# Optimization experiments

Hardware: AMD Instinct MI355X
Metric: run time of the kernel (lower is better)

Reference implementation:

```python
import jax, jax.numpy as jnp
import numpy as np

N_NODES = 200_000
N_EDGES = 6_400_000
N_GRAPHS = 512


def _graph_conv(x, src, dst, W_rel, b_rel, W_root, n_nodes):
    # PyG GraphConv (aggr='add'): lin_rel(sum_{j->i} x_j) + lin_root(x_i)
    agg = jax.ops.segment_sum(x[src], dst, num_segments=n_nodes)  # [N, in]
    return agg @ W_rel.T + b_rel + x @ W_root.T


def setup_inputs() -> dict:
    key = jax.random.key(0)
    ks = jax.random.split(key, 12)
    x = jax.random.normal(ks[0], (N_NODES, 3), dtype=jnp.float32)
    edge_index = jax.random.randint(ks[1], (2, N_EDGES), 0, N_NODES, dtype=jnp.int64)
    batch = jnp.sort(jax.random.randint(ks[2], (N_NODES,), 0, N_GRAPHS, dtype=jnp.int64))

    def xavier(k, shape):
        fan_out, fan_in = shape
        lim = np.sqrt(6.0 / (fan_in + fan_out)).astype(np.float32)
        return jax.random.uniform(k, shape, jnp.float32, -lim, lim)

    return {
        "x": x, "edge_index": edge_index, "batch": batch,
        "W1_rel": xavier(ks[3], (32, 3)),  "b1": jnp.zeros((32,), jnp.float32), "W1_root": xavier(ks[4], (32, 3)),
        "W2_rel": xavier(ks[5], (16, 32)), "b2": jnp.zeros((16,), jnp.float32), "W2_root": xavier(ks[6], (16, 32)),
        "W3_rel": xavier(ks[7], (8, 16)),  "b3": jnp.zeros((8,), jnp.float32),  "W3_root": xavier(ks[8], (8, 16)),
        "W_lin": xavier(ks[9], (1, 8)),    "b_lin": jnp.zeros((1,), jnp.float32),
    }


def reference(x, edge_index, batch,
              W1_rel, b1, W1_root,
              W2_rel, b2, W2_root,
              W3_rel, b3, W3_root,
              W_lin, b_lin):
    src, dst = edge_index[0], edge_index[1]
    h = jax.nn.relu(_graph_conv(x, src, dst, W1_rel, b1, W1_root, N_NODES))
    h = jax.nn.relu(_graph_conv(h, src, dst, W2_rel, b2, W2_root, N_NODES))
    h = jax.nn.relu(_graph_conv(h, src, dst, W3_rel, b3, W3_root, N_NODES))
    pooled = jax.ops.segment_max(h, batch, num_segments=N_GRAPHS)  # [G, 8]
    out = pooled @ W_lin.T + b_lin  # [G, 1]
    return out[:, 0]
```

## Files before the change

### kernel.cpp

```cpp
#include <hip/hip_runtime.h>
#include <hip/hip_fp16.h>

#define N_NODES 200000
#define N_EDGES 6400000
#define N_GRAPHS 512

#define NB1 196
#define CB 1024
#define NSB 16
#define NFB (NB1 * NSB)
#define CHUNK 8192
#define NCH 782
#define NGRP 25
#define CPG 32
#define SCAP 3072

typedef float vf4 __attribute__((ext_vector_type(4)));
typedef float vf2 __attribute__((ext_vector_type(2)));
typedef unsigned vu2 __attribute__((ext_vector_type(2)));

__device__ __forceinline__ unsigned ntload_u(const unsigned* p) {
  return __builtin_nontemporal_load(p);
}
__device__ __forceinline__ int ntload_i(const int* p) { return __builtin_nontemporal_load(p); }
__device__ __forceinline__ float ntload_f(const float* p) {
  return __builtin_nontemporal_load(p);
}
__device__ __forceinline__ float2 ntload_f2(const float* p) {
  vf2 v = __builtin_nontemporal_load((const vf2*)p);
  return make_float2(v.x, v.y);
}
__device__ __forceinline__ void ntstore_f2(float* p, float2 v) {
  vf2 t = {v.x, v.y};
  __builtin_nontemporal_store(t, (vf2*)p);
}
__device__ __forceinline__ void ntstore_u(unsigned* p, unsigned v) {
  __builtin_nontemporal_store(v, p);
}


__global__ __launch_bounds__(256) void count_kernel(const int* __restrict__ dst,
                                                    unsigned short* __restrict__ H) {
  __shared__ unsigned hist[4][NB1];
  int t = threadIdx.x, w = t >> 6;
  for (int i = t; i < 4 * NB1; i += 256) ((unsigned*)hist)[i] = 0;
  __syncthreads();
  int c = blockIdx.x;
  long e0 = (long)c * CHUNK;
  long rem = (long)N_EDGES - e0;
  int n = rem > CHUNK ? CHUNK : (int)rem;
  for (int i = t; i < n; i += 256) atomicAdd(&hist[w][dst[e0 + i] >> 10], 1u);
  __syncthreads();
  for (int b = t; b < NB1; b += 256)
    H[(size_t)c * NB1 + b] =
        (unsigned short)(hist[0][b] + hist[1][b] + hist[2][b] + hist[3][b]);
}

__global__ __launch_bounds__(256) void scan_bins1_kernel(unsigned short* __restrict__ H,
                                                         unsigned* __restrict__ P) {
  int b = blockIdx.x * 256 + threadIdx.x;
  int g = blockIdx.y;
  if (b >= NB1) return;
  int c0 = g * CPG, c1 = min(NCH, (g + 1) * CPG);
  unsigned run = 0;
  for (int c = c0; c < c1; c++) {
    unsigned t = H[(size_t)c * NB1 + b];
    H[(size_t)c * NB1 + b] = (unsigned short)run;
    run += t;
  }
  P[(size_t)g * NB1 + b] = run;
}

__global__ __launch_bounds__(256) void scan_bins2_kernel(unsigned* __restrict__ P,
                                                         unsigned* __restrict__ bucketTotal) {
  int b = blockIdx.x * 256 + threadIdx.x;
  if (b >= NB1) return;
  unsigned run = 0;
  for (int g = 0; g < NGRP; g++) {
    unsigned t = P[(size_t)g * NB1 + b];
    P[(size_t)g * NB1 + b] = run;
    run += t;
  }
  bucketTotal[b] = run;
}

__global__ __launch_bounds__(256) void scan_total_kernel(const unsigned* __restrict__ bucketTotal,
                                                         unsigned* __restrict__ bucketStart) {
  __shared__ unsigned partial[256];
  int t = threadIdx.x;
  unsigned v = (t < NB1) ? bucketTotal[t] : 0u;
  partial[t] = v;
  __syncthreads();
  for (int off = 1; off < 256; off <<= 1) {
    unsigned add = (t >= off) ? partial[t - off] : 0u;
    __syncthreads();
    partial[t] += add;
    __syncthreads();
  }
  if (t < NB1) bucketStart[t] = partial[t] - v;
  if (t == 0) bucketStart[NB1] = N_EDGES;
}

__global__ __launch_bounds__(256) void scatterA_kernel(
    const int* __restrict__ src, const int* __restrict__ dst,
    const unsigned short* __restrict__ H, const unsigned* __restrict__ P,
    const unsigned* __restrict__ bucketStart, unsigned* __restrict__ X1) {
  __shared__ unsigned ssort[CHUNK];
  __shared__ unsigned char sbort[CHUNK];
  __shared__ unsigned histw[4][NB1];
  __shared__ unsigned curw[4][NB1];
  __shared__ unsigned gbase[NB1];
  __shared__ unsigned partial[256];
  int t = threadIdx.x, w = t >> 6;
  int c = blockIdx.x;
  int g = c / CPG;
  long e0 = (long)c * CHUNK;
  long rem = (long)N_EDGES - e0;
  int n = rem > CHUNK ? CHUNK : (int)rem;
  for (int i = t; i < 4 * NB1; i += 256) ((unsigned*)histw)[i] = 0;
  __syncthreads();
  for (int i = t; i < n; i += 256) atomicAdd(&histw[w][dst[e0 + i] >> 10], 1u);
  __syncthreads();
  unsigned tot = 0, h0 = 0, h1 = 0, h2 = 0, h3 = 0;
  if (t < NB1) {
    h0 = histw[0][t]; h1 = histw[1][t]; h2 = histw[2][t]; h3 = histw[3][t];
    tot = h0 + h1 + h2 + h3;
  }
  partial[t] = tot;
  __syncthreads();
  for (int off = 1; off < 256; off <<= 1) {
    unsigned add = (t >= off) ? partial[t - off] : 0u;
    __syncthreads();
    partial[t] += add;
    __syncthreads();
  }
  if (t < NB1) {
    unsigned ex = partial[t] - tot;
    unsigned r = ex;
    curw[0][t] = r; r += h0;
    curw[1][t] = r; r += h1;
    curw[2][t] = r; r += h2;
    curw[3][t] = r;
    gbase[t] = bucketStart[t] + P[(size_t)g * NB1 + t] + (unsigned)H[(size_t)c * NB1 + t] - ex;
  }
  __syncthreads();
  for (int i = t; i < n; i += 256) {
    int d = dst[e0 + i], s = src[e0 + i];
    int b = d >> 10;
    unsigned r = atomicAdd(&curw[w][b], 1u);
    ssort[r] = ((unsigned)s << 10) | (unsigned)(d & 1023);
    sbort[r] = (unsigned char)b;
  }
  __syncthreads();
  for (int j = t; j < n; j += 256) X1[gbase[sbort[j]] + j] = ssort[j];
}

__global__ __launch_bounds__(1024) void scatterB_kernel(
    const unsigned* __restrict__ X1, const unsigned* __restrict__ bucketStart,
    unsigned* __restrict__ X2, unsigned* __restrict__ fineStart) {
  __shared__ unsigned histw[16][NSB];
  __shared__ unsigned binstart[NSB + 1];
  __shared__ unsigned cur[NSB];
  int t = threadIdx.x, w = t >> 6, b = blockIdx.x;
  unsigned cs0 = bucketStart[b], cs1 = bucketStart[b + 1];
  int n = (int)(cs1 - cs0);
  if (t < 16 * NSB) ((unsigned*)histw)[t] = 0;
  __syncthreads();
  for (int i = t; i < n; i += 1024)
    atomicAdd(&histw[w][(X1[cs0 + i] >> 6) & 15u], 1u);
  __syncthreads();
  if (t == 0) {
    unsigned run = 0;
    for (int k = 0; k < NSB; k++) {
      binstart[k] = run;
      unsigned tot = 0;
      for (int ww = 0; ww < 16; ww++) tot += histw[ww][k];
      run += tot;
    }
    binstart[NSB] = run;
  }
  __syncthreads();
  if (t < NSB) {
    fineStart[b * NSB + t] = cs0 + binstart[t];
    cur[t] = binstart[t];
  }
  if (b == NB1 - 1 && t == 0) fineStart[NFB] = cs1;
  __syncthreads();
  for (int i = t; i < n; i += 1024) {
    unsigned v = X1[cs0 + i];
    unsigned pos = atomicAdd(&cur[(v >> 6) & 15u], 1u);
    X2[cs0 + pos] = v;
  }
}

__global__ __launch_bounds__(256) void sort2_kernel(const unsigned* __restrict__ X2,
                                                    const unsigned* __restrict__ fineStart,
                                                    unsigned* __restrict__ packedB,
                                                    unsigned* __restrict__ nodeStart) {
  __shared__ unsigned buf[SCAP];
  __shared__ unsigned buf2[SCAP];
  __shared__ unsigned hist[64], base[64], cur[64];
  int t = threadIdx.x, b = blockIdx.x;
  unsigned s0 = fineStart[b], s1 = fineStart[b + 1];
  int n = (int)(s1 - s0);
  if (t < 64) hist[t] = 0;
  for (int i = t; i < n; i += 256) buf[i] = ntload_u(&X2[s0 + i]);
  __syncthreads();
  for (int i = t; i < n; i += 256) atomicAdd(&hist[buf[i] & 63u], 1u);
  __syncthreads();
  if (t == 0) {
    unsigned run = 0;
    for (int k = 0; k < 64; k++) {
      unsigned v = hist[k];
      base[k] = run;
      cur[k] = run;
      run += v;
    }
  }
  __syncthreads();
  if (t < 64) {
    int gn = b * 64 + t;
    if (gn <= N_NODES) nodeStart[gn] = s0 + base[t];
  }
  for (int i = t; i < n; i += 256) {
    unsigned p = buf[i];
    unsigned pos = atomicAdd(&cur[p & 63u], 1u);
    buf2[pos] = p >> 10;
  }
  __syncthreads();
  for (int i = t; i < n; i += 256) ntstore_u(&packedB[s0 + i], buf2[i]);
}

__global__ __launch_bounds__(256) void xpad_kernel(const float* __restrict__ x,
                                                   float4* __restrict__ xp) {
  int n = blockIdx.x * 256 + threadIdx.x;
  if (n >= N_NODES) return;
  xp[n] = make_float4(x[3 * n], x[3 * n + 1], x[3 * n + 2], 0.f);
}

__device__ __forceinline__ void half8_unpack(uint4 g, float* f) {
  const __half2* h2 = reinterpret_cast<const __half2*>(&g);
#pragma unroll
  for (int j = 0; j < 4; j++) {
    float2 fj = __half22float2(h2[j]);
    f[2 * j] = fj.x;
    f[2 * j + 1] = fj.y;
  }
}

__global__ __launch_bounds__(256) void layer1a_kernel(
    const unsigned* __restrict__ packed, const unsigned* __restrict__ nodeStart,
    const float4* __restrict__ xp, float* __restrict__ agg) {
  int t = threadIdx.x, ln = t >> 2, part = t & 3;
  int node = blockIdx.x * 64 + ln;
  unsigned s1v = ntload_u(&nodeStart[node + 1]);
  float a0 = 0.f, a1 = 0.f, a2 = 0.f;
  for (unsigned base = ntload_u(&nodeStart[node]) + part; base < s1v; base += 16) {
    unsigned i1 = base + 4, i2 = base + 8, i3 = base + 12;
    unsigned e0 = ntload_u(&packed[base]);
    unsigned e1 = ntload_u(&packed[i1]);
    unsigned e2 = ntload_u(&packed[i2]);
    unsigned e3 = ntload_u(&packed[i3]);
    float4 g0 = xp[e0], g1 = xp[e1], g2 = xp[e2], g3 = xp[e3];
    float m1 = (i1 < s1v) ? 1.f : 0.f;
    float m2 = (i2 < s1v) ? 1.f : 0.f;
    float m3 = (i3 < s1v) ? 1.f : 0.f;
    a0 += g0.x + m1 * g1.x + m2 * g2.x + m3 * g3.x;
    a1 += g0.y + m1 * g1.y + m2 * g2.y + m3 * g3.y;
    a2 += g0.z + m1 * g1.z + m2 * g2.z + m3 * g3.z;
  }
  a0 += __shfl_xor(a0, 1); a1 += __shfl_xor(a1, 1); a2 += __shfl_xor(a2, 1);
  a0 += __shfl_xor(a0, 2); a1 += __shfl_xor(a1, 2); a2 += __shfl_xor(a2, 2);
  float v = (part == 0) ? a0 : (part == 1) ? a1 : (part == 2) ? a2 : 0.f;
  agg[(size_t)node * 4 + part] = v;
}

__global__ __launch_bounds__(256) void layer1b_kernel(
    const float4* __restrict__ xp, const float4* __restrict__ agg,
    const float* __restrict__ W1_rel, const float* __restrict__ b1,
    const float* __restrict__ W1_root,
    const float* __restrict__ W2_rel, const float* __restrict__ W2_root,
    uint4* __restrict__ t2h4, float4* __restrict__ r24) {
  __shared__ float sW1rel[96], sW1root[96], sb1[32], sW2rel[512], sW2root[512];
  for (int i = threadIdx.x; i < 96; i += 256) { sW1rel[i] = W1_rel[i]; sW1root[i] = W1_root[i]; }
  for (int i = threadIdx.x; i < 32; i += 256) sb1[i] = b1[i];
  for (int i = threadIdx.x; i < 512; i += 256) { sW2rel[i] = W2_rel[i]; sW2root[i] = W2_root[i]; }
  __syncthreads();
  int node = blockIdx.x * 256 + threadIdx.x;
  if (node >= N_NODES) return;
  float4 A = agg[node];
  float4 xv = xp[node];
  float h[32];
#pragma unroll
  for (int k = 0; k < 32; k++) {
    float v = sW1rel[3 * k] * A.x + sW1rel[3 * k + 1] * A.y + sW1rel[3 * k + 2] * A.z +
              sW1root[3 * k] * xv.x + sW1root[3 * k + 1] * xv.y + sW1root[3 * k + 2] * xv.z +
              sb1[k];
    h[k] = fmaxf(v, 0.f);
  }
  unsigned tp[8];
#pragma unroll
  for (int j = 0; j < 16; j += 2) {
    float t0 = 0.f, t1 = 0.f;
#pragma unroll
    for (int k = 0; k < 32; k++) {
      t0 += sW2rel[32 * j + k] * h[k];
      t1 += sW2rel[32 * (j + 1) + k] * h[k];
    }
    __half2 pk = __halves2half2(__float2half_rn(t0), __float2half_rn(t1));
    tp[j >> 1] = *(unsigned*)&pk;
  }
  t2h4[(size_t)node * 2] = make_uint4(tp[0], tp[1], tp[2], tp[3]);
  t2h4[(size_t)node * 2 + 1] = make_uint4(tp[4], tp[5], tp[6], tp[7]);
#pragma unroll
  for (int q = 0; q < 4; q++) {
    float rv[4];
#pragma unroll
    for (int jj = 0; jj < 4; jj++) {
      int j = 4 * q + jj;
      float a = 0.f;
#pragma unroll
      for (int k = 0; k < 32; k++) a += sW2root[32 * j + k] * h[k];
      rv[jj] = a;
    }
    r24[(size_t)node * 4 + q] = make_float4(rv[0], rv[1], rv[2], rv[3]);
  }
}

__global__ __launch_bounds__(256) void layer2_kernel(
    const unsigned* __restrict__ packed, const unsigned* __restrict__ nodeStart,
    const uint4* __restrict__ t2h4, const float* __restrict__ r2,
    const float* __restrict__ b2,
    const float* __restrict__ W3_rel, const float* __restrict__ W3_root,
    unsigned* __restrict__ t3h, float* __restrict__ r3) {
  __shared__ float sW3rel[128], sW3root[128], sb2[16];
  __shared__ float plds[256 * 9];
  __shared__ float hlds[32 * 16];
  for (int i = threadIdx.x; i < 128; i += 256) { sW3rel[i] = W3_rel[i]; sW3root[i] = W3_root[i]; }
  if (threadIdx.x < 16) sb2[threadIdx.x] = b2[threadIdx.x];
  __syncthreads();
  int t = threadIdx.x, ln = t >> 3, p = t & 7;
  int node = blockIdx.x * 32 + ln;
  int half = p & 1;
  unsigned s1v = ntload_u(&nodeStart[node + 1]);
  float acc[8];
#pragma unroll
  for (int j = 0; j < 8; j++) acc[j] = 0.f;
  for (unsigned base = ntload_u(&nodeStart[node]) + (p >> 1); base < s1v; base += 16) {
    unsigned i1 = base + 4, i2 = base + 8, i3 = base + 12;
    unsigned e0 = ntload_u(&packed[base]);
    unsigned e1 = ntload_u(&packed[i1]);
    unsigned e2 = ntload_u(&packed[i2]);
    unsigned e3 = ntload_u(&packed[i3]);
    uint4 g0 = t2h4[(size_t)e0 * 2 + half];
    uint4 g1 = t2h4[(size_t)e1 * 2 + half];
    uint4 g2 = t2h4[(size_t)e2 * 2 + half];
    uint4 g3 = t2h4[(size_t)e3 * 2 + half];
    float m1 = (i1 < s1v) ? 1.f : 0.f;
    float m2 = (i2 < s1v) ? 1.f : 0.f;
    float m3 = (i3 < s1v) ? 1.f : 0.f;
    float f0[8], f1[8], f2[8], f3[8];
    half8_unpack(g0, f0);
    half8_unpack(g1, f1);
    half8_unpack(g2, f2);
    half8_unpack(g3, f3);
#pragma unroll
    for (int j = 0; j < 8; j++)
      acc[j] += f0[j] + m1 * f1[j] + m2 * f2[j] + m3 * f3[j];
  }
#pragma unroll
  for (int j = 0; j < 8; j++) plds[t * 9 + j] = acc[j];
  __syncthreads();
  {
    float2 rv = ntload_f2(&r2[(size_t)node * 16 + 2 * p]);
    float hv[2];
#pragma unroll
    for (int k2 = 0; k2 < 2; k2++) {
      int f = 2 * p + k2;
      int fh = f >> 3, fi = f & 7;
      int q0 = (ln * 8 + fh) * 9 + fi;
      float s = plds[q0] + plds[q0 + 18] + plds[q0 + 36] + plds[q0 + 54];
      hv[k2] = s + sb2[f] + (k2 == 0 ? rv.x : rv.y);
    }
    hlds[ln * 16 + 2 * p] = fmaxf(hv[0], 0.f);
    hlds[ln * 16 + 2 * p + 1] = fmaxf(hv[1], 0.f);
  }
  __syncthreads();
  const float* W = (p < 4) ? sW3rel : sW3root;
  int rbase = (p < 4) ? 2 * p : 2 * (p - 4);
  float o0 = 0.f, o1 = 0.f;
#pragma unroll
  for (int k = 0; k < 16; k++) {
    float hv = hlds[ln * 16 + k];
    o0 += W[16 * rbase + k] * hv;
    o1 += W[16 * (rbase + 1) + k] * hv;
  }
  if (p < 4) {
    __half2 pk = __halves2half2(__float2half_rn(o0), __float2half_rn(o1));
    t3h[(size_t)node * 4 + p] = *(unsigned*)&pk;
  } else {
    ntstore_f2(&r3[(size_t)node * 8 + rbase], make_float2(o0, o1));
  }
}

__global__ __launch_bounds__(256) void layer3_kernel(
    const unsigned* __restrict__ packed, const unsigned* __restrict__ nodeStart,
    const uint4* __restrict__ t3h4, const float* __restrict__ r3,
    const float* __restrict__ b3,
    const int* __restrict__ batch, unsigned* __restrict__ pooled) {
  __shared__ float plds[256 * 9];
  __shared__ float sb3[8];
  __shared__ int sgid[32];
  if (threadIdx.x < 8) sb3[threadIdx.x] = b3[threadIdx.x];
  __syncthreads();
  int t = threadIdx.x, ln = t >> 3, p = t & 7;
  int node = blockIdx.x * 32 + ln;
  unsigned s1v = ntload_u(&nodeStart[node + 1]);
  float acc[8];
#pragma unroll
  for (int j = 0; j < 8; j++) acc[j] = 0.f;
  for (unsigned base = ntload_u(&nodeStart[node]) + p; base < s1v; base += 32) {
    unsigned i1 = base + 8, i2 = base + 16, i3 = base + 24;
    unsigned e0 = ntload_u(&packed[base]);
    unsigned e1 = ntload_u(&packed[i1]);
    unsigned e2 = ntload_u(&packed[i2]);
    unsigned e3 = ntload_u(&packed[i3]);
    uint4 g0 = t3h4[e0];
    uint4 g1 = t3h4[e1];
    uint4 g2 = t3h4[e2];
    uint4 g3 = t3h4[e3];
    float m1 = (i1 < s1v) ? 1.f : 0.f;
    float m2 = (i2 < s1v) ? 1.f : 0.f;
    float m3 = (i3 < s1v) ? 1.f : 0.f;
    float f0[8], f1[8], f2[8], f3[8];
    half8_unpack(g0, f0);
    half8_unpack(g1, f1);
    half8_unpack(g2, f2);
    half8_unpack(g3, f3);
#pragma unroll
    for (int j = 0; j < 8; j++)
      acc[j] += f0[j] + m1 * f1[j] + m2 * f2[j] + m3 * f3[j];
  }
#pragma unroll
  for (int j = 0; j < 8; j++) plds[t * 9 + j] = acc[j];
  __syncthreads();
  int gg = ntload_i(&batch[node]);
  int q0 = ln * 72 + p;
  float v = plds[q0] + plds[q0 + 9] + plds[q0 + 18] + plds[q0 + 27] +
            plds[q0 + 36] + plds[q0 + 45] + plds[q0 + 54] + plds[q0 + 63];
  float h = fmaxf(v + sb3[p] + ntload_f(&r3[(size_t)node * 8 + p]), 0.f);
  __syncthreads();
  plds[ln * 9 + p] = h;
  if (p == 0) sgid[ln] = gg;
  __syncthreads();
  if (t < 8) {
    int gcur = sgid[0];
    float m = plds[t];
    for (int l = 1; l < 32; l++) {
      int g2 = sgid[l];
      float hv = plds[l * 9 + t];
      if (g2 != gcur) {
        atomicMax(&pooled[8 * gcur + t], __float_as_uint(m));
        gcur = g2;
        m = hv;
      } else {
        m = fmaxf(m, hv);
      }
    }
    atomicMax(&pooled[8 * gcur + t], __float_as_uint(m));
  }
}

__global__ __launch_bounds__(256) void final_kernel(
    const unsigned* __restrict__ pooled, const float* __restrict__ W_lin,
    const float* __restrict__ b_lin, float* __restrict__ out) {
  int g = blockIdx.x * blockDim.x + threadIdx.x;
  if (g >= N_GRAPHS) return;
  float acc = b_lin[0];
#pragma unroll
  for (int f = 0; f < 8; f++) acc += __uint_as_float(pooled[8 * g + f]) * W_lin[f];
  out[g] = acc;
}

extern "C" void kernel_launch(void* const* d_in, const int* in_sizes, int n_in,
                              void* d_out, int out_size, void* d_ws, size_t ws_size,
                              hipStream_t stream) {
  const float* x = (const float*)d_in[0];
  const int* ei = (const int*)d_in[1];
  const int* src = ei;
  const int* dst = ei + N_EDGES;
  const int* batch = (const int*)d_in[2];
  const float* W1_rel = (const float*)d_in[3];
  const float* b1 = (const float*)d_in[4];
  const float* W1_root = (const float*)d_in[5];
  const float* W2_rel = (const float*)d_in[6];
  const float* b2 = (const float*)d_in[7];
  const float* W2_root = (const float*)d_in[8];
  const float* W3_rel = (const float*)d_in[9];
  const float* b3 = (const float*)d_in[10];
  const float* W3_root = (const float*)d_in[11];
  const float* W_lin = (const float*)d_in[12];
  const float* b_lin = (const float*)d_in[13];
  float* out = (float*)d_out;

  char* ws = (char*)d_ws;
  unsigned* X2 = (unsigned*)(ws + 0);
  float* r2 = (float*)(ws + 0);
  float* agg = (float*)(ws + 12800000);
  float* r3 = (float*)(ws + 12800000);
  unsigned* t3h = (unsigned*)(ws + 19200000);
  float4* xpad = (float4*)(ws + 22400000);
  unsigned* X1 = (unsigned*)(ws + 25600000);
  unsigned* packedB = (unsigned*)(ws + 25600000);
  unsigned* t2h = (unsigned*)(ws + 51200128);
  unsigned short* H = (unsigned short*)(ws + 51200128);
  unsigned* P = (unsigned*)(ws + 51506672);
  unsigned* bucketTotal = (unsigned*)(ws + 51526272);
  unsigned* bucketStart = (unsigned*)(ws + 51527056);
  unsigned* fineStart = (unsigned*)(ws + 51527844);
  unsigned* pooled = (unsigned*)(ws + 57600128);
  unsigned* nodeStart = (unsigned*)(ws + 57954016);

  hipMemsetAsync(pooled, 0, N_GRAPHS * 8 * sizeof(unsigned), stream);
  hipMemsetAsync(packedB + N_EDGES, 0, 128, stream);

  count_kernel<<<NCH, 256, 0, stream>>>(dst, H);
  scan_bins1_kernel<<<dim3((NB1 + 255) / 256, NGRP), 256, 0, stream>>>(H, P);
  scan_bins2_kernel<<<(NB1 + 255) / 256, 256, 0, stream>>>(P, bucketTotal);
  scan_total_kernel<<<1, 256, 0, stream>>>(bucketTotal, bucketStart);
  scatterA_kernel<<<NCH, 256, 0, stream>>>(src, dst, H, P, bucketStart, X1);
  scatterB_kernel<<<NB1, 1024, 0, stream>>>(X1, bucketStart, X2, fineStart);
  sort2_kernel<<<NFB, 256, 0, stream>>>(X2, fineStart, packedB, nodeStart);
  xpad_kernel<<<(N_NODES + 255) / 256, 256, 0, stream>>>(x, xpad);

  layer1a_kernel<<<N_NODES / 64, 256, 0, stream>>>(packedB, nodeStart, xpad, agg);
  layer1b_kernel<<<(N_NODES + 255) / 256, 256, 0, stream>>>(
      xpad, (const float4*)agg, W1_rel, b1, W1_root, W2_rel, W2_root,
      (uint4*)t2h, (float4*)r2);
  layer2_kernel<<<N_NODES / 32, 256, 0, stream>>>(packedB, nodeStart, (const uint4*)t2h, r2, b2,
                                                  W3_rel, W3_root, t3h, r3);
  layer3_kernel<<<N_NODES / 32, 256, 0, stream>>>(packedB, nodeStart, (const uint4*)t3h, r3, b3,
                                                  batch, pooled);
  final_kernel<<<(N_GRAPHS + 255) / 256, 256, 0, stream>>>(pooled, W_lin, b_lin, out);
}
```

Baseline: 429.0 us.

## Split layer-2 gather by feature half and move epilogue to separate kernel

Layer 2 is split into two kernels. The gather kernel now has each block handle only one 8-feature half of the 16-wide half-precision table, with blocks ordered so both halves of the same node group run close together. Each thread walks every 8th edge and the block writes fp16 partial aggregates. A separate elementwise kernel then applies bias, residual and ReLU, and computes the layer-3 projections. The aim is to shrink the gathered footprint per block and improve cache locality, at the cost of reading the edge list twice, one extra launch and an fp16 round-trip of the aggregate.

```diff
diff --git a/kernel.cpp b/kernel.cpp
--- a/kernel.cpp
+++ b/kernel.cpp
@@ -14,6 +14,7 @@
 #define NGRP 25
 #define CPG 32
 #define SCAP 3072
+#define NBLK32 (N_NODES / 32)
 
 typedef float vf4 __attribute__((ext_vector_type(4)));
 typedef float vf2 __attribute__((ext_vector_type(2)));
@@ -327,27 +328,22 @@
   }
 }
 
-__global__ __launch_bounds__(256) void layer2_kernel(
+__global__ __launch_bounds__(256) void layer2g_kernel(
     const unsigned* __restrict__ packed, const unsigned* __restrict__ nodeStart,
-    const uint4* __restrict__ t2h4, const float* __restrict__ r2,
-    const float* __restrict__ b2,
-    const float* __restrict__ W3_rel, const float* __restrict__ W3_root,
-    unsigned* __restrict__ t3h, float* __restrict__ r3) {
-  __shared__ float sW3rel[128], sW3root[128], sb2[16];
+    const uint4* __restrict__ t2h4, __half* __restrict__ agg2) {
   __shared__ float plds[256 * 9];
-  __shared__ float hlds[32 * 16];
-  for (int i = threadIdx.x; i < 128; i += 256) { sW3rel[i] = W3_rel[i]; sW3root[i] = W3_root[i]; }
-  if (threadIdx.x < 16) sb2[threadIdx.x] = b2[threadIdx.x];
-  __syncthreads();
   int t = threadIdx.x, ln = t >> 3, p = t & 7;
-  int node = blockIdx.x * 32 + ln;
-  int half = p & 1;
+  int b = blockIdx.x;
+  int r = b & 7, half = r & 1, sub = r >> 1;
+  int nodeblk = (b >> 3) * 4 + sub;
+  if (nodeblk >= NBLK32) return;
+  int node = nodeblk * 32 + ln;
   unsigned s1v = ntload_u(&nodeStart[node + 1]);
   float acc[8];
 #pragma unroll
   for (int j = 0; j < 8; j++) acc[j] = 0.f;
-  for (unsigned base = ntload_u(&nodeStart[node]) + (p >> 1); base < s1v; base += 16) {
-    unsigned i1 = base + 4, i2 = base + 8, i3 = base + 12;
+  for (unsigned base = ntload_u(&nodeStart[node]) + p; base < s1v; base += 32) {
+    unsigned i1 = base + 8, i2 = base + 16, i3 = base + 24;
     unsigned e0 = ntload_u(&packed[base]);
     unsigned e1 = ntload_u(&packed[i1]);
     unsigned e2 = ntload_u(&packed[i2]);
@@ -371,36 +367,59 @@
 #pragma unroll
   for (int j = 0; j < 8; j++) plds[t * 9 + j] = acc[j];
   __syncthreads();
-  {
-    float2 rv = ntload_f2(&r2[(size_t)node * 16 + 2 * p]);
-    float hv[2];
-#pragma unroll
-    for (int k2 = 0; k2 < 2; k2++) {
-      int f = 2 * p + k2;
-      int fh = f >> 3, fi = f & 7;
-      int q0 = (ln * 8 + fh) * 9 + fi;
-      float s = plds[q0] + plds[q0 + 18] + plds[q0 + 36] + plds[q0 + 54];
-      hv[k2] = s + sb2[f] + (k2 == 0 ? rv.x : rv.y);
+  int q0 = ln * 72 + p;
+  float s = plds[q0] + plds[q0 + 9] + plds[q0 + 18] + plds[q0 + 27] +
+            plds[q0 + 36] + plds[q0 + 45] + plds[q0 + 54] + plds[q0 + 63];
+  agg2[(size_t)node * 16 + half * 8 + p] = __float2half_rn(s);
+}
+
+__global__ __launch_bounds__(256) void layer2e_kernel(
+    const uint4* agg2q, const float4* __restrict__ r24,
+    const float* __restrict__ b2, const float* __restrict__ W3_rel,
+    const float* __restrict__ W3_root, uint4* __restrict__ t3h4, float4* r34) {
+  __shared__ float sW3rel[128], sW3root[128], sb2[16];
+  for (int i = threadIdx.x; i < 128; i += 256) { sW3rel[i] = W3_rel[i]; sW3root[i] = W3_root[i]; }
+  if (threadIdx.x < 16) sb2[threadIdx.x] = b2[threadIdx.x];
+  __syncthreads();
+  int node = blockIdx.x * 256 + threadIdx.x;
+  if (node >= N_NODES) return;
+  uint4 ga = agg2q[(size_t)node * 2];
+  uint4 gb = agg2q[(size_t)node * 2 + 1];
+  float ag[16];
+  half8_unpack(ga, ag);
+  half8_unpack(gb, ag + 8);
+  float h[16];
+#pragma unroll
+  for (int q = 0; q < 4; q++) {
+    float4 rv = r24[(size_t)node * 4 + q];
+    h[4 * q] = fmaxf(ag[4 * q] + rv.x + sb2[4 * q], 0.f);
+    h[4 * q + 1] = fmaxf(ag[4 * q + 1] + rv.y + sb2[4 * q + 1], 0.f);
+    h[4 * q + 2] = fmaxf(ag[4 * q + 2] + rv.z + sb2[4 * q + 2], 0.f);
+    h[4 * q + 3] = fmaxf(ag[4 * q + 3] + rv.w + sb2[4 * q + 3], 0.f);
+  }
+  unsigned tp[4];
+#pragma unroll
+  for (int j = 0; j < 8; j += 2) {
+    float t0 = 0.f, t1 = 0.f;
+#pragma unroll
+    for (int k = 0; k < 16; k++) {
+      t0 += sW3rel[16 * j + k] * h[k];
+      t1 += sW3rel[16 * (j + 1) + k] * h[k];
     }
-    hlds[ln * 16 + 2 * p] = fmaxf(hv[0], 0.f);
-    hlds[ln * 16 + 2 * p + 1] = fmaxf(hv[1], 0.f);
-  }
-  __syncthreads();
-  const float* W = (p < 4) ? sW3rel : sW3root;
-  int rbase = (p < 4) ? 2 * p : 2 * (p - 4);
-  float o0 = 0.f, o1 = 0.f;
-#pragma unroll
-  for (int k = 0; k < 16; k++) {
-    float hv = hlds[ln * 16 + k];
-    o0 += W[16 * rbase + k] * hv;
-    o1 += W[16 * (rbase + 1) + k] * hv;
-  }
-  if (p < 4) {
-    __half2 pk = __halves2half2(__float2half_rn(o0), __float2half_rn(o1));
-    t3h[(size_t)node * 4 + p] = *(unsigned*)&pk;
-  } else {
-    ntstore_f2(&r3[(size_t)node * 8 + rbase], make_float2(o0, o1));
-  }
+    __half2 pk = __halves2half2(__float2half_rn(t0), __float2half_rn(t1));
+    tp[j >> 1] = *(unsigned*)&pk;
+  }
+  t3h4[node] = make_uint4(tp[0], tp[1], tp[2], tp[3]);
+  float rv[8];
+#pragma unroll
+  for (int j = 0; j < 8; j++) {
+    float a = 0.f;
+#pragma unroll
+    for (int k = 0; k < 16; k++) a += sW3root[16 * j + k] * h[k];
+    rv[j] = a;
+  }
+  r34[(size_t)node * 2] = make_float4(rv[0], rv[1], rv[2], rv[3]);
+  r34[(size_t)node * 2 + 1] = make_float4(rv[4], rv[5], rv[6], rv[7]);
 }
 
 __global__ __launch_bounds__(256) void layer3_kernel(
@@ -507,6 +526,7 @@
   unsigned* X2 = (unsigned*)(ws + 0);
   float* r2 = (float*)(ws + 0);
   float* agg = (float*)(ws + 12800000);
+  __half* agg2 = (__half*)(ws + 12800000);
   float* r3 = (float*)(ws + 12800000);
   unsigned* t3h = (unsigned*)(ws + 19200000);
   float4* xpad = (float4*)(ws + 22400000);
@@ -537,8 +557,13 @@
   layer1b_kernel<<<(N_NODES + 255) / 256, 256, 0, stream>>>(
       xpad, (const float4*)agg, W1_rel, b1, W1_root, W2_rel, W2_root,
       (uint4*)t2h, (float4*)r2);
-  layer2_kernel<<<N_NODES / 32, 256, 0, stream>>>(packedB, nodeStart, (const uint4*)t2h, r2, b2,
-                                                  W3_rel, W3_root, t3h, r3);
+
+  layer2g_kernel<<<((NBLK32 + 3) / 4) * 8, 256, 0, stream>>>(
+      packedB, nodeStart, (const uint4*)t2h, agg2);
+  layer2e_kernel<<<(N_NODES + 255) / 256, 256, 0, stream>>>(
+      (const uint4*)agg2, (const float4*)r2, b2, W3_rel, W3_root,
+      (uint4*)t3h, (float4*)r3);
+
   layer3_kernel<<<N_NODES / 32, 256, 0, stream>>>(packedB, nodeStart, (const uint4*)t3h, r3, b3,
                                                   batch, pooled);
   final_kernel<<<(N_GRAPHS + 255) / 256, 256, 0, stream>>>(pooled, W_lin, b_lin, out);
```

After: 492.0 us. +14.7%, slower.
